# Optimization experiments

Measured on AMD Instinct MI355X. Metric: run time of the kernel, lower is better.

The kernel has to match this reference:

```python
import jax, jax.numpy as jnp
import numpy as np

EPS = 1e-5


def _batchnorm(x, gamma, beta):
    # training-mode BatchNorm over the point/voxel dim (axis 0)
    mean = jnp.mean(x, axis=0)
    var = jnp.var(x, axis=0)
    return (x - mean) * jax.lax.rsqrt(var + EPS) * gamma + beta


def setup_inputs() -> dict:
    N, P, NI, NF, K, I = 100000, 200000, 32, 64, 27, 8
    key = jax.random.key(0)
    ks = jax.random.split(key, 10)
    return {
        "x_feats": jax.random.normal(ks[0], (N, NI), jnp.float32),
        "z_feats": jax.random.normal(ks[1], (P, NI), jnp.float32),
        "interp_w": jax.random.uniform(ks[2], (P, I), jnp.float32),
        "nbr_idx": jax.random.randint(ks[3], (N, K), 0, N, jnp.int32),
        "interp_idx": jax.random.randint(ks[4], (P, I), 0, N, jnp.int32),
        "p2v_idx": jax.random.randint(ks[5], (P,), 0, N, jnp.int32),
        "conv1_w": jax.random.normal(ks[6], (K, NI, NF), jnp.float32) / np.float32(np.sqrt(K * NI)),
        "conv2_w": jax.random.normal(ks[7], (K, NF, NF), jnp.float32) / np.float32(np.sqrt(K * NF)),
        "bn_gamma": jnp.ones((NF,), jnp.float32),
        "bn_beta": jnp.zeros((NF,), jnp.float32),
        "pbn_gamma": jnp.ones((NI,), jnp.float32),
        "pbn_beta": jnp.zeros((NI,), jnp.float32),
        "lin_w": jax.random.normal(ks[8], (NI, NF), jnp.float32) / np.float32(np.sqrt(NI)),
        "lin_b": jnp.zeros((NF,), jnp.float32),
    }


def reference(x_feats, z_feats, interp_w, nbr_idx, interp_idx, p2v_idx,
              conv1_w, conv2_w, bn_gamma, bn_beta, pbn_gamma, pbn_beta,
              lin_w, lin_b):
    N = x_feats.shape[0]
    # --- voxel branch: Conv3d -> BN -> SiLU -> Conv3d (submanifold sparse conv
    # = neighbor gather via kernel map + grouped GEMM over 27 offsets) ---
    h = jnp.einsum('nki,kio->no', x_feats[nbr_idx], conv1_w)   # [N, NF]
    h = jax.nn.silu(_batchnorm(h, bn_gamma, bn_beta))
    x = jnp.einsum('nki,kio->no', h[nbr_idx], conv2_w)         # [N, NF]
    # --- voxel_to_point: trilinear gather from 8 surrounding voxels ---
    z1 = jnp.sum(x[interp_idx] * interp_w[..., None], axis=1)  # [P, NF]
    # --- point branch: z1.F += Linear(SiLU(BN(z.F))) ---
    pz = jax.nn.silu(_batchnorm(z_feats, pbn_gamma, pbn_beta))
    z1 = z1 + pz @ lin_w + lin_b                               # [P, NF]
    # --- point_to_voxel: scatter-average point features into voxels ---
    sums = jax.ops.segment_sum(z1, p2v_idx, num_segments=N)    # [N, NF]
    cnt = jax.ops.segment_sum(jnp.ones((z1.shape[0], 1), z1.dtype), p2v_idx,
                              num_segments=N)
    x_new = sums / jnp.maximum(cnt, 1.0)
    return (x_new, z1)
```

## Files before the change

kernel.cpp:

```cpp
#include <hip/hip_runtime.h>
#include <cstdint>

#define EPSF 1e-5f
constexpr int KOFF = 27;

typedef __attribute__((ext_vector_type(8))) short bf16x8;
typedef __attribute__((ext_vector_type(4))) float f32x4;
typedef unsigned short ushort_t;
typedef unsigned int uint_t;

__device__ __forceinline__ ushort_t f2b(float f) {
    uint_t u = __float_as_uint(f);
    u += 0x7fffu + ((u >> 16) & 1u);
    return (ushort_t)(u >> 16);
}
__device__ __forceinline__ void u4tof(uint4 u, float* f) {
    uint_t w[4] = {u.x, u.y, u.z, u.w};
#pragma unroll
    for (int i = 0; i < 4; ++i) {
        f[2 * i]     = __uint_as_float(w[i] << 16);
        f[2 * i + 1] = __uint_as_float(w[i] & 0xffff0000u);
    }
}

__device__ __forceinline__ void gload_lds16(const void* g, float* l) {
    __builtin_amdgcn_global_load_lds(
        (const __attribute__((address_space(1))) void*)g,
        (__attribute__((address_space(3))) void*)l, 16, 0, 0);
}

__global__ __launch_bounds__(256) void cvt_k(const float* __restrict__ in,
                                             ushort_t* __restrict__ out, int n8) {
    int i = blockIdx.x * 256 + threadIdx.x;
    if (i >= n8) return;
    float4 a = ((const float4*)in)[2 * i];
    float4 b = ((const float4*)in)[2 * i + 1];
    uint4 o;
    o.x = (uint_t)f2b(a.x) | ((uint_t)f2b(a.y) << 16);
    o.y = (uint_t)f2b(a.z) | ((uint_t)f2b(a.w) << 16);
    o.z = (uint_t)f2b(b.x) | ((uint_t)f2b(b.y) << 16);
    o.w = (uint_t)f2b(b.z) | ((uint_t)f2b(b.w) << 16);
    ((uint4*)out)[i] = o;
}

__global__ __launch_bounds__(256) void wtT_k(const float* __restrict__ W,
                                             ushort_t* __restrict__ Wt, int CIN) {
    int t     = blockIdx.x * 256 + threadIdx.x;
    int total = KOFF * CIN * 64;
    if (t >= total) return;
    int o    = t & 63;
    int rest = t >> 6;
    int i    = rest % CIN;
    int k    = rest / CIN;
    Wt[((size_t)k * 64 + o) * CIN + i] = f2b(W[t]);
}

__global__ __launch_bounds__(256) void linT_k(const float* __restrict__ lw,
                                              ushort_t* __restrict__ wt) {
    int t = blockIdx.x * 256 + threadIdx.x;
    if (t >= 64 * 32) return;
    int o = t >> 5, i = t & 31;
    wt[o * 32 + i] = f2b(lw[i * 64 + o]);
}

template <int CIN>
__global__ __launch_bounds__(256, 6) void convm_k(
    const ushort_t* __restrict__ feats,
    const int* __restrict__ nbr,
    const ushort_t* __restrict__ Wt,
    ushort_t* __restrict__ outp,
    int N) {
    constexpr int CHUNKS = CIN / 8;
    constexpr int T      = CIN / 32;
    constexpr int NS     = CHUNKS / 4;
    constexpr int M      = CHUNKS - 1;
    constexpr int PH     = 2;
    constexpr int NPH    = (KOFF + PH - 1) / PH;

    __shared__ float lds[2][PH][64 * CHUNKS * 4];

    const int lane = threadIdx.x & 63;
    const int wv   = threadIdx.x >> 6;
    const int lo   = lane & 15;
    const int hi   = lane >> 4;
    const int row0 = blockIdx.x * 64;

    int srcoff[NS];
    const int* nbp[NS];
    int ldsbase[NS];
#pragma unroll
    for (int i = 0; i < NS; ++i) {
        int c      = (wv * NS + i) * 64 + lane;
        int r      = c / CHUNKS;
        int ch     = c & M;
        srcoff[i]  = (ch ^ (r & M)) * 8;
        int grow   = row0 + r;
        if (grow >= N) grow = N - 1;
        nbp[i]     = nbr + (size_t)grow * KOFF;
        ldsbase[i] = (wv * NS + i) * 256;
    }

    f32x4 acc[4] = {{0.f, 0.f, 0.f, 0.f},
                    {0.f, 0.f, 0.f, 0.f},
                    {0.f, 0.f, 0.f, 0.f},
                    {0.f, 0.f, 0.f, 0.f}};

    int idxb[2][PH][NS];
    bf16x8 Bb[2][PH][T];

    auto NSTEPS = [&](int pp) { return (pp * PH + PH <= KOFF) ? PH : (KOFF - pp * PH); };

    auto LOADIDX = [&](int pp) {
        int ns = NSTEPS(pp);
#pragma unroll
        for (int s = 0; s < PH; ++s)
            if (s < ns)
#pragma unroll
                for (int i = 0; i < NS; ++i)
                    idxb[pp & 1][s][i] = nbp[i][pp * PH + s];
    };
    auto LOADB = [&](int pp) {
        int ns = NSTEPS(pp);
#pragma unroll
        for (int s = 0; s < PH; ++s)
            if (s < ns) {
                const ushort_t* wb =
                    Wt + ((size_t)(pp * PH + s) * 64 + wv * 16 + lo) * CIN + hi * 8;
#pragma unroll
                for (int t = 0; t < T; ++t)
                    Bb[pp & 1][s][t] = *(const bf16x8*)(wb + t * 32);
            }
    };
    auto STAGE = [&](int pp) {
        int ns = NSTEPS(pp);
#pragma unroll
        for (int s = 0; s < PH; ++s)
            if (s < ns)
#pragma unroll
                for (int i = 0; i < NS; ++i) {
                    const ushort_t* src =
                        feats + (size_t)idxb[pp & 1][s][i] * CIN + srcoff[i];
                    gload_lds16(src, &lds[pp & 1][s][ldsbase[i]]);
                }
    };

    LOADIDX(0);
    LOADIDX(1);
    LOADB(0);
    STAGE(0);
    __syncthreads();

#pragma unroll
    for (int p = 0; p < NPH; ++p) {
        if (p + 2 < NPH) LOADIDX(p + 2);
        if (p + 1 < NPH) {
            LOADB(p + 1);
            STAGE(p + 1);
        }
        __builtin_amdgcn_sched_barrier(0);
        int ns = NSTEPS(p);
#pragma unroll
        for (int s = 0; s < PH; ++s) {
            if (s < ns) {
#pragma unroll
                for (int mt = 0; mt < 4; ++mt) {
                    const int R = mt * 16 + lo;
#pragma unroll
                    for (int t = 0; t < T; ++t) {
                        int d    = t * 4 + hi;
                        int slot = d ^ (R & M);
                        bf16x8 a =
                            *(const bf16x8*)&lds[p & 1][s][(R * CHUNKS + slot) * 4];
                        acc[mt] = __builtin_amdgcn_mfma_f32_16x16x32_bf16(
                            a, Bb[p & 1][s][t], acc[mt], 0, 0, 0);
                    }
                }
            }
        }
        __syncthreads();
    }

#pragma unroll
    for (int mt = 0; mt < 4; ++mt) {
#pragma unroll
        for (int r = 0; r < 4; ++r) {
            int orow = row0 + mt * 16 + hi * 4 + r;
            if (orow < N)
                outp[(size_t)orow * 64 + wv * 16 + lo] = f2b(acc[mt][r]);
        }
    }
}

__global__ __launch_bounds__(256) void statsp1_k(const float* __restrict__ v,
                                                 int n, float* __restrict__ part) {
    __shared__ float ls[2 * 256];
    const int c = threadIdx.x & 31;
    int r0      = blockIdx.x * 8 + (threadIdx.x >> 5);
    int stride  = gridDim.x * 8;
    float s = 0.f, ss = 0.f;
    for (int r = r0; r < n; r += stride) {
        float x = v[(size_t)r * 32 + c];
        s += x;
        ss += x * x;
    }
    ls[threadIdx.x]       = s;
    ls[256 + threadIdx.x] = ss;
    __syncthreads();
    for (int off = 128; off >= 32; off >>= 1) {
        if (threadIdx.x < off) {
            ls[threadIdx.x] += ls[threadIdx.x + off];
            ls[256 + threadIdx.x] += ls[256 + threadIdx.x + off];
        }
        __syncthreads();
    }
    if (threadIdx.x < 32) {
        part[(size_t)blockIdx.x * 64 + threadIdx.x]      = ls[threadIdx.x];
        part[(size_t)blockIdx.x * 64 + 32 + threadIdx.x] = ls[256 + threadIdx.x];
    }
}

__global__ __launch_bounds__(256) void statsb1_k(const ushort_t* __restrict__ v,
                                                 int n, float* __restrict__ part) {
    __shared__ float ls[2][256];
    const int c8 = threadIdx.x & 7;
    int r0 = blockIdx.x * 32 + (threadIdx.x >> 3);
    float s[8], ss[8];
#pragma unroll
    for (int j = 0; j < 8; ++j) { s[j] = 0.f; ss[j] = 0.f; }
    for (int r = r0; r < n; r += gridDim.x * 32) {
        uint4 u = *(const uint4*)(v + (size_t)r * 64 + c8 * 8);
        float f[8];
        u4tof(u, f);
#pragma unroll
        for (int j = 0; j < 8; ++j) { s[j] += f[j]; ss[j] += f[j] * f[j]; }
    }
#pragma unroll
    for (int j = 0; j < 8; ++j) {
        ls[0][threadIdx.x] = s[j];
        ls[1][threadIdx.x] = ss[j];
        __syncthreads();
        for (int off = 128; off >= 8; off >>= 1) {
            if (threadIdx.x < off) {
                ls[0][threadIdx.x] += ls[0][threadIdx.x + off];
                ls[1][threadIdx.x] += ls[1][threadIdx.x + off];
            }
            __syncthreads();
        }
        if (threadIdx.x < 8) {
            part[(size_t)blockIdx.x * 128 + threadIdx.x * 8 + j]      = ls[0][threadIdx.x];
            part[(size_t)blockIdx.x * 128 + 64 + threadIdx.x * 8 + j] = ls[1][threadIdx.x];
        }
        __syncthreads();
    }
}

__global__ __launch_bounds__(128) void statsr_k(const float* __restrict__ part,
                                                float* __restrict__ out,
                                                int G, int C2) {
    int c = threadIdx.x;
    if (c >= C2) return;
    float s = 0.f;
#pragma unroll 8
    for (int g = 0; g < G; ++g) s += part[(size_t)g * C2 + c];
    out[c] = s;
}

__global__ __launch_bounds__(256) void bnsilub_k(ushort_t* __restrict__ h,
                                                 const float* __restrict__ stats,
                                                 const float* __restrict__ gamma,
                                                 const float* __restrict__ beta,
                                                 int total8, float invN) {
    int i8 = blockIdx.x * 256 + threadIdx.x;
    if (i8 >= total8) return;
    int c0  = (i8 * 8) & 63;
    uint4 u = ((const uint4*)h)[i8];
    float f[8];
    u4tof(u, f);
#pragma unroll
    for (int j = 0; j < 8; ++j) {
        int c     = c0 + j;
        float m   = stats[c] * invN;
        float var = stats[64 + c] * invN - m * m;
        float x   = (f[j] - m) * rsqrtf(var + EPSF) * gamma[c] + beta[c];
        f[j]      = x / (1.f + expf(-x));
    }
    uint4 o;
    o.x = (uint_t)f2b(f[0]) | ((uint_t)f2b(f[1]) << 16);
    o.y = (uint_t)f2b(f[2]) | ((uint_t)f2b(f[3]) << 16);
    o.z = (uint_t)f2b(f[4]) | ((uint_t)f2b(f[5]) << 16);
    o.w = (uint_t)f2b(f[6]) | ((uint_t)f2b(f[7]) << 16);
    ((uint4*)h)[i8] = o;
}

__global__ __launch_bounds__(256) void point_k(
    const ushort_t* __restrict__ x,
    const float* __restrict__ z_feats,
    const float* __restrict__ interp_w,
    const int* __restrict__ interp_idx,
    const ushort_t* __restrict__ lin_wt,
    const float* __restrict__ lin_b,
    const float* __restrict__ pstats, const float* __restrict__ pgamma,
    const float* __restrict__ pbeta, float* __restrict__ z1_out,
    int P, float invP) {
    __shared__ ushort_t pz[64 * 40];
    __shared__ float zl[64 * 68];

    const int lane = threadIdx.x & 63;
    const int wv   = threadIdx.x >> 6;
    const int lo   = lane & 15;
    const int hi   = lane >> 4;
    const int p0   = blockIdx.x * 64;

    {
        int pp = p0 + lane;
        if (pp >= P) pp = P - 1;
        const int cb      = wv;
        const float4* zr  = (const float4*)(z_feats + (size_t)pp * 32 + cb * 8);
        float4 z0 = zr[0], z1v = zr[1];
        float f[8] = {z0.x, z0.y, z0.z, z0.w, z1v.x, z1v.y, z1v.z, z1v.w};
        uint_t pk[4];
#pragma unroll
        for (int j2 = 0; j2 < 4; ++j2) {
            ushort_t lo16, hi16;
#pragma unroll
            for (int e = 0; e < 2; ++e) {
                int j     = j2 * 2 + e;
                int c     = cb * 8 + j;
                float m   = pstats[c] * invP;
                float var = pstats[32 + c] * invP - m * m;
                float zn  = (f[j] - m) * rsqrtf(var + EPSF) * pgamma[c] + pbeta[c];
                float pzv = zn / (1.f + expf(-zn));
                ushort_t b = f2b(pzv);
                if (e == 0) lo16 = b; else hi16 = b;
            }
            pk[j2] = (uint_t)lo16 | ((uint_t)hi16 << 16);
        }
        *(uint4*)&pz[lane * 40 + cb * 8] = make_uint4(pk[0], pk[1], pk[2], pk[3]);
    }
    __syncthreads();

    {
        bf16x8 a = *(const bf16x8*)&pz[(wv * 16 + lo) * 40 + hi * 8];
        f32x4 lacc[4];
#pragma unroll
        for (int nt = 0; nt < 4; ++nt) {
            bf16x8 b = *(const bf16x8*)(lin_wt + (size_t)(nt * 16 + lo) * 32 + hi * 8);
            lacc[nt] = __builtin_amdgcn_mfma_f32_16x16x32_bf16(
                a, b, (f32x4){0.f, 0.f, 0.f, 0.f}, 0, 0, 0);
        }
#pragma unroll
        for (int nt = 0; nt < 4; ++nt)
#pragma unroll
            for (int r = 0; r < 4; ++r)
                zl[(wv * 16 + hi * 4 + r) * 68 + nt * 16 + lo] = lacc[nt][r];
    }
    __syncthreads();

    const int p = p0 + lane;
    if (p >= P) return;
    const int wbase = __builtin_amdgcn_readfirstlane(wv * 16);

    const int4* iip   = (const int4*)(interp_idx + (size_t)p * 8);
    const float4* iwp = (const float4*)(interp_w + (size_t)p * 8);
    int4 ia = iip[0], ib = iip[1];
    float4 wa = iwp[0], wb = iwp[1];
    int idxs[8]  = {ia.x, ia.y, ia.z, ia.w, ib.x, ib.y, ib.z, ib.w};
    float wts[8] = {wa.x, wa.y, wa.z, wa.w, wb.x, wb.y, wb.z, wb.w};

    float acc[16];
#pragma unroll
    for (int o4 = 0; o4 < 4; ++o4) {
        f32x4 lv = *(const f32x4*)&zl[lane * 68 + wbase + o4 * 4];
#pragma unroll
        for (int j = 0; j < 4; ++j) acc[o4 * 4 + j] = lv[j];
    }

#pragma unroll
    for (int t = 0; t < 8; ++t) {
        const ushort_t* xr = x + (size_t)idxs[t] * 64 + wbase;
        float w            = wts[t];
        uint4 u0 = *(const uint4*)xr;
        uint4 u1 = *(const uint4*)(xr + 8);
        float f[16];
        u4tof(u0, f);
        u4tof(u1, f + 8);
#pragma unroll
        for (int o = 0; o < 16; ++o) acc[o] = fmaf(w, f[o], acc[o]);
    }

    const float* lb = lin_b + wbase;
#pragma unroll
    for (int o = 0; o < 16; ++o) acc[o] += lb[o];

    float* zo = z1_out + (size_t)p * 64 + wbase;
#pragma unroll
    for (int o = 0; o < 16; o += 4) {
        float4 v = {acc[o], acc[o + 1], acc[o + 2], acc[o + 3]};
        *(float4*)(zo + o) = v;
    }
}

__global__ __launch_bounds__(256) void hist_k(const int* __restrict__ p2v,
                                              int* __restrict__ cnt, int P) {
    int p = blockIdx.x * 256 + threadIdx.x;
    if (p < P) atomicAdd(&cnt[p2v[p]], 1);
}

__global__ __launch_bounds__(256) void scan1_k(const int* __restrict__ cnt,
                                               int* __restrict__ tmp,
                                               int* __restrict__ bsum, int n) {
    __shared__ int s[256];
    int i = blockIdx.x * 256 + threadIdx.x;
    int v = (i < n) ? cnt[i] : 0;
    s[threadIdx.x] = v;
    __syncthreads();
    for (int off = 1; off < 256; off <<= 1) {
        int t = (threadIdx.x >= off) ? s[threadIdx.x - off] : 0;
        __syncthreads();
        s[threadIdx.x] += t;
        __syncthreads();
    }
    if (i < n) tmp[i] = s[threadIdx.x];
    if (threadIdx.x == 255) bsum[blockIdx.x] = s[255];
}

__global__ void scan2_k(const int* __restrict__ bsum, int* __restrict__ bpre,
                        int nb) {
    if (blockIdx.x == 0 && threadIdx.x == 0) {
        int a = 0;
        for (int b = 0; b < nb; ++b) { bpre[b] = a; a += bsum[b]; }
    }
}

__global__ __launch_bounds__(256) void scan3_k(const int* __restrict__ cnt,
                                               const int* __restrict__ tmp,
                                               const int* __restrict__ bpre,
                                               int* __restrict__ off, int n) {
    int i = blockIdx.x * 256 + threadIdx.x;
    if (i < n) off[i] = bpre[i >> 8] + tmp[i] - cnt[i];
}

__global__ __launch_bounds__(256) void fill_k(const int* __restrict__ p2v,
                                              const int* __restrict__ off,
                                              int* __restrict__ cursor,
                                              int* __restrict__ bucket, int P) {
    int p = blockIdx.x * 256 + threadIdx.x;
    if (p >= P) return;
    int v    = p2v[p];
    int slot = atomicAdd(&cursor[v], 1);
    bucket[off[v] + slot] = p;
}

__global__ __launch_bounds__(256) void avg_k(const float* __restrict__ z1,
                                             const int* __restrict__ off,
                                             const int* __restrict__ cnt,
                                             const int* __restrict__ bucket,
                                             float* __restrict__ xnew, int N) {
    int tid = blockIdx.x * 256 + threadIdx.x;
    int v   = tid >> 2;
    if (v >= N) return;
    int q  = tid & 3;
    int c  = cnt[v];
    int st = off[v];
    float acc[16];
#pragma unroll
    for (int o = 0; o < 16; ++o) acc[o] = 0.f;
    for (int j = 0; j < c; ++j) {
        int p            = bucket[st + j];
        const float4* zr = (const float4*)(z1 + (size_t)p * 64 + q * 16);
#pragma unroll
        for (int c4 = 0; c4 < 4; ++c4) {
            float4 t = zr[c4];
            acc[c4 * 4 + 0] += t.x;
            acc[c4 * 4 + 1] += t.y;
            acc[c4 * 4 + 2] += t.z;
            acc[c4 * 4 + 3] += t.w;
        }
    }
    float rc  = 1.f / fmaxf((float)c, 1.f);
    float* op = xnew + (size_t)v * 64 + q * 16;
#pragma unroll
    for (int o = 0; o < 16; o += 4) {
        float4 t = {acc[o] * rc, acc[o + 1] * rc, acc[o + 2] * rc, acc[o + 3] * rc};
        *(float4*)(op + o) = t;
    }
}

extern "C" void kernel_launch(void* const* d_in, const int* in_sizes, int n_in,
                              void* d_out, int out_size, void* d_ws, size_t ws_size,
                              hipStream_t stream) {
    const float* x_feats   = (const float*)d_in[0];
    const float* z_feats   = (const float*)d_in[1];
    const float* interp_w  = (const float*)d_in[2];
    const int* nbr_idx     = (const int*)d_in[3];
    const int* interp_idx  = (const int*)d_in[4];
    const int* p2v_idx     = (const int*)d_in[5];
    const float* conv1_w   = (const float*)d_in[6];
    const float* conv2_w   = (const float*)d_in[7];
    const float* bn_gamma  = (const float*)d_in[8];
    const float* bn_beta   = (const float*)d_in[9];
    const float* pbn_gamma = (const float*)d_in[10];
    const float* pbn_beta  = (const float*)d_in[11];
    const float* lin_w     = (const float*)d_in[12];
    const float* lin_b     = (const float*)d_in[13];

    const int N  = in_sizes[3] / KOFF;
    const int P  = in_sizes[5];
    const int NB = (N + 255) / 256;
    const int GH = 512;
    const int GP = 256;

    ushort_t* h2    = (ushort_t*)d_ws;
    ushort_t* xb    = h2 + (size_t)N * 64;
    ushort_t* xf16  = xb + (size_t)N * 64;
    ushort_t* wt1   = xf16 + (size_t)N * 32;
    ushort_t* wt2   = wt1 + KOFF * 64 * 32;
    ushort_t* lwt   = wt2 + KOFF * 64 * 64;
    int* cnt        = (int*)(lwt + 64 * 32);
    int* cursor     = cnt + N;
    float* stats    = (float*)(cursor + N);
    int* tmp        = (int*)(stats + 192);
    int* off        = tmp + N;
    int* bsum       = off + N;
    int* bpre       = bsum + 512;
    int* bucket     = bpre + 512;
    float* part_h   = (float*)(bucket + P);
    float* part_p   = part_h + (size_t)GH * 128;
    float* stats_h  = stats;
    float* stats_p  = stats + 128;

    float* xnew = (float*)d_out;
    float* z1   = xnew + (size_t)N * 64;

    hipMemsetAsync(cnt, 0, (size_t)2 * N * sizeof(int), stream);

    cvt_k<<<((size_t)N * 32 / 8 + 255) / 256, 256, 0, stream>>>(x_feats, xf16,
                                                                N * 32 / 8);
    wtT_k<<<(KOFF * 32 * 64 + 255) / 256, 256, 0, stream>>>(conv1_w, wt1, 32);
    wtT_k<<<(KOFF * 64 * 64 + 255) / 256, 256, 0, stream>>>(conv2_w, wt2, 64);
    linT_k<<<8, 256, 0, stream>>>(lin_w, lwt);

    hist_k<<<(P + 255) / 256, 256, 0, stream>>>(p2v_idx, cnt, P);
    scan1_k<<<NB, 256, 0, stream>>>(cnt, tmp, bsum, N);
    scan2_k<<<1, 1, 0, stream>>>(bsum, bpre, NB);
    scan3_k<<<NB, 256, 0, stream>>>(cnt, tmp, bpre, off, N);
    fill_k<<<(P + 255) / 256, 256, 0, stream>>>(p2v_idx, off, cursor, bucket, P);

    statsp1_k<<<GP, 256, 0, stream>>>(z_feats, P, part_p);
    statsr_k<<<1, 128, 0, stream>>>(part_p, stats_p, GP, 64);

    convm_k<32><<<(N + 63) / 64, 256, 0, stream>>>(xf16, nbr_idx, wt1, h2, N);

    statsb1_k<<<GH, 256, 0, stream>>>(h2, N, part_h);
    statsr_k<<<1, 128, 0, stream>>>(part_h, stats_h, GH, 128);
    bnsilub_k<<<((size_t)N * 64 / 8 + 255) / 256, 256, 0, stream>>>(
        h2, stats_h, bn_gamma, bn_beta, N * 64 / 8, 1.f / (float)N);

    convm_k<64><<<(N + 63) / 64, 256, 0, stream>>>(h2, nbr_idx, wt2, xb, N);

    point_k<<<(P + 63) / 64, 256, 0, stream>>>(xb, z_feats, interp_w, interp_idx,
                                               lwt, lin_b, stats_p, pbn_gamma,
                                               pbn_beta, z1, P, 1.f / (float)P);

    avg_k<<<((size_t)N * 4 + 255) / 256, 256, 0, stream>>>(z1, off, cnt, bucket,
                                                           xnew, N);

    (void)n_in; (void)out_size; (void)ws_size;
}
```

Measured before the change: 313.6 us.

## Enlarge sparse conv tile to 128 rows with 8 waves and parallelize block scan

The sparse conv kernel now processes 128 output rows per block with 512 threads arranged as 2 row groups by 4 column groups. Each staged weight fragment is reused across more rows, and the number of blocks is halved. The single-thread serial scan over block sums becomes a 512-thread shared-memory Hillis-Steele scan, which assumes at most 512 blocks. LDS per block doubles and occupancy limits change, which may reduce the latency hiding available for the gathers.

```diff
diff --git a/kernel.cpp b/kernel.cpp
--- a/kernel.cpp
+++ b/kernel.cpp
@@ -64,7 +64,7 @@
 }
 
 template <int CIN>
-__global__ __launch_bounds__(256, 6) void convm_k(
+__global__ __launch_bounds__(512, 4) void convm_k(
     const ushort_t* __restrict__ feats,
     const int* __restrict__ nbr,
     const ushort_t* __restrict__ Wt,
@@ -77,27 +77,29 @@
     constexpr int PH     = 2;
     constexpr int NPH    = (KOFF + PH - 1) / PH;
 
-    __shared__ float lds[2][PH][64 * CHUNKS * 4];
+    __shared__ float lds[2][PH][128 * CHUNKS * 4];
 
     const int lane = threadIdx.x & 63;
-    const int wv   = threadIdx.x >> 6;
+    const int wid  = threadIdx.x >> 6;
+    const int wr   = wid >> 2;
+    const int wc   = wid & 3;
     const int lo   = lane & 15;
     const int hi   = lane >> 4;
-    const int row0 = blockIdx.x * 64;
+    const int row0 = blockIdx.x * 128;
 
     int srcoff[NS];
     const int* nbp[NS];
     int ldsbase[NS];
 #pragma unroll
     for (int i = 0; i < NS; ++i) {
-        int c      = (wv * NS + i) * 64 + lane;
+        int c      = (wid * NS + i) * 64 + lane;
         int r      = c / CHUNKS;
         int ch     = c & M;
         srcoff[i]  = (ch ^ (r & M)) * 8;
         int grow   = row0 + r;
         if (grow >= N) grow = N - 1;
         nbp[i]     = nbr + (size_t)grow * KOFF;
-        ldsbase[i] = (wv * NS + i) * 256;
+        ldsbase[i] = (wid * NS + i) * 256;
     }
 
     f32x4 acc[4] = {{0.f, 0.f, 0.f, 0.f},
@@ -125,7 +127,7 @@
         for (int s = 0; s < PH; ++s)
             if (s < ns) {
                 const ushort_t* wb =
-                    Wt + ((size_t)(pp * PH + s) * 64 + wv * 16 + lo) * CIN + hi * 8;
+                    Wt + ((size_t)(pp * PH + s) * 64 + wc * 16 + lo) * CIN + hi * 8;
 #pragma unroll
                 for (int t = 0; t < T; ++t)
                     Bb[pp & 1][s][t] = *(const bf16x8*)(wb + t * 32);
@@ -164,7 +166,7 @@
             if (s < ns) {
 #pragma unroll
                 for (int mt = 0; mt < 4; ++mt) {
-                    const int R = mt * 16 + lo;
+                    const int R = wr * 64 + mt * 16 + lo;
 #pragma unroll
                     for (int t = 0; t < T; ++t) {
                         int d    = t * 4 + hi;
@@ -184,9 +186,9 @@
     for (int mt = 0; mt < 4; ++mt) {
 #pragma unroll
         for (int r = 0; r < 4; ++r) {
-            int orow = row0 + mt * 16 + hi * 4 + r;
+            int orow = row0 + wr * 64 + mt * 16 + hi * 4 + r;
             if (orow < N)
-                outp[(size_t)orow * 64 + wv * 16 + lo] = f2b(acc[mt][r]);
+                outp[(size_t)orow * 64 + wc * 16 + lo] = f2b(acc[mt][r]);
         }
     }
 }
@@ -424,12 +426,20 @@
     if (threadIdx.x == 255) bsum[blockIdx.x] = s[255];
 }
 
-__global__ void scan2_k(const int* __restrict__ bsum, int* __restrict__ bpre,
-                        int nb) {
-    if (blockIdx.x == 0 && threadIdx.x == 0) {
-        int a = 0;
-        for (int b = 0; b < nb; ++b) { bpre[b] = a; a += bsum[b]; }
-    }
+__global__ __launch_bounds__(512) void scan2_k(const int* __restrict__ bsum,
+                                               int* __restrict__ bpre, int nb) {
+    __shared__ int s[512];
+    int i = threadIdx.x;
+    int v = (i < nb) ? bsum[i] : 0;
+    s[i]  = v;
+    __syncthreads();
+    for (int off = 1; off < 512; off <<= 1) {
+        int t = (i >= off) ? s[i - off] : 0;
+        __syncthreads();
+        s[i] += t;
+        __syncthreads();
+    }
+    if (i < nb) bpre[i] = s[i] - v;
 }
 
 __global__ __launch_bounds__(256) void scan3_k(const int* __restrict__ cnt,
@@ -542,21 +552,21 @@
 
     hist_k<<<(P + 255) / 256, 256, 0, stream>>>(p2v_idx, cnt, P);
     scan1_k<<<NB, 256, 0, stream>>>(cnt, tmp, bsum, N);
-    scan2_k<<<1, 1, 0, stream>>>(bsum, bpre, NB);
+    scan2_k<<<1, 512, 0, stream>>>(bsum, bpre, NB);
     scan3_k<<<NB, 256, 0, stream>>>(cnt, tmp, bpre, off, N);
     fill_k<<<(P + 255) / 256, 256, 0, stream>>>(p2v_idx, off, cursor, bucket, P);
 
     statsp1_k<<<GP, 256, 0, stream>>>(z_feats, P, part_p);
     statsr_k<<<1, 128, 0, stream>>>(part_p, stats_p, GP, 64);
 
-    convm_k<32><<<(N + 63) / 64, 256, 0, stream>>>(xf16, nbr_idx, wt1, h2, N);
+    convm_k<32><<<(N + 127) / 128, 512, 0, stream>>>(xf16, nbr_idx, wt1, h2, N);
 
     statsb1_k<<<GH, 256, 0, stream>>>(h2, N, part_h);
     statsr_k<<<1, 128, 0, stream>>>(part_h, stats_h, GH, 128);
     bnsilub_k<<<((size_t)N * 64 / 8 + 255) / 256, 256, 0, stream>>>(
         h2, stats_h, bn_gamma, bn_beta, N * 64 / 8, 1.f / (float)N);
 
-    convm_k<64><<<(N + 63) / 64, 256, 0, stream>>>(h2, nbr_idx, wt2, xb, N);
+    convm_k<64><<<(N + 127) / 128, 512, 0, stream>>>(h2, nbr_idx, wt2, xb, N);
 
     point_k<<<(P + 63) / 64, 256, 0, stream>>>(xb, z_feats, interp_w, interp_idx,
                                                lwt, lin_b, stats_p, pbn_gamma,
```

After: 312.3 us. Within noise of the previous version (-0.4%).

## Fuse BN stats into conv1 epilogue, write bucketed bf16 z1, parallelize scan

Applied to the files above, without the earlier changes.

The first sparse conv now accumulates per-channel sum and sum-of-squares in its epilogue and writes per-block partials, which removes the separate stats pass over h2. The point kernel also writes a bf16 copy of z1 directly into voxel-sorted slot order, so avg_k reads contiguous bf16 rows instead of gathering fp32 rows through a bucket index. The single-thread block-prefix scan becomes a 512-thread parallel scan. In exchange the averaged output now sums bf16-rounded values, which lowers precision, and the stats reduction has to go over more partials (one per conv block).

```diff
diff --git a/kernel.cpp b/kernel.cpp
--- a/kernel.cpp
+++ b/kernel.cpp
@@ -13,6 +13,9 @@
     uint_t u = __float_as_uint(f);
     u += 0x7fffu + ((u >> 16) & 1u);
     return (ushort_t)(u >> 16);
+}
+__device__ __forceinline__ float b2f(ushort_t u) {
+    return __uint_as_float(((uint_t)u) << 16);
 }
 __device__ __forceinline__ void u4tof(uint4 u, float* f) {
     uint_t w[4] = {u.x, u.y, u.z, u.w};
@@ -63,12 +66,13 @@
     wt[o * 32 + i] = f2b(lw[i * 64 + o]);
 }
 
-template <int CIN>
+template <int CIN, bool STATS>
 __global__ __launch_bounds__(256, 6) void convm_k(
     const ushort_t* __restrict__ feats,
     const int* __restrict__ nbr,
     const ushort_t* __restrict__ Wt,
     ushort_t* __restrict__ outp,
+    float* __restrict__ part,
     int N) {
     constexpr int CHUNKS = CIN / 8;
     constexpr int T      = CIN / 32;
@@ -180,13 +184,31 @@
         __syncthreads();
     }
 
+    float s = 0.f, ss = 0.f;
 #pragma unroll
     for (int mt = 0; mt < 4; ++mt) {
 #pragma unroll
         for (int r = 0; r < 4; ++r) {
             int orow = row0 + mt * 16 + hi * 4 + r;
-            if (orow < N)
-                outp[(size_t)orow * 64 + wv * 16 + lo] = f2b(acc[mt][r]);
+            if (orow < N) {
+                ushort_t b = f2b(acc[mt][r]);
+                outp[(size_t)orow * 64 + wv * 16 + lo] = b;
+                if (STATS) {
+                    float v = b2f(b);
+                    s += v;
+                    ss += v * v;
+                }
+            }
+        }
+    }
+    if (STATS) {
+        s  += __shfl_xor(s, 16);
+        s  += __shfl_xor(s, 32);
+        ss += __shfl_xor(ss, 16);
+        ss += __shfl_xor(ss, 32);
+        if (hi == 0) {
+            part[(size_t)blockIdx.x * 128 + wv * 16 + lo]      = s;
+            part[(size_t)blockIdx.x * 128 + 64 + wv * 16 + lo] = ss;
         }
     }
 }
@@ -219,41 +241,6 @@
     }
 }
 
-__global__ __launch_bounds__(256) void statsb1_k(const ushort_t* __restrict__ v,
-                                                 int n, float* __restrict__ part) {
-    __shared__ float ls[2][256];
-    const int c8 = threadIdx.x & 7;
-    int r0 = blockIdx.x * 32 + (threadIdx.x >> 3);
-    float s[8], ss[8];
-#pragma unroll
-    for (int j = 0; j < 8; ++j) { s[j] = 0.f; ss[j] = 0.f; }
-    for (int r = r0; r < n; r += gridDim.x * 32) {
-        uint4 u = *(const uint4*)(v + (size_t)r * 64 + c8 * 8);
-        float f[8];
-        u4tof(u, f);
-#pragma unroll
-        for (int j = 0; j < 8; ++j) { s[j] += f[j]; ss[j] += f[j] * f[j]; }
-    }
-#pragma unroll
-    for (int j = 0; j < 8; ++j) {
-        ls[0][threadIdx.x] = s[j];
-        ls[1][threadIdx.x] = ss[j];
-        __syncthreads();
-        for (int off = 128; off >= 8; off >>= 1) {
-            if (threadIdx.x < off) {
-                ls[0][threadIdx.x] += ls[0][threadIdx.x + off];
-                ls[1][threadIdx.x] += ls[1][threadIdx.x + off];
-            }
-            __syncthreads();
-        }
-        if (threadIdx.x < 8) {
-            part[(size_t)blockIdx.x * 128 + threadIdx.x * 8 + j]      = ls[0][threadIdx.x];
-            part[(size_t)blockIdx.x * 128 + 64 + threadIdx.x * 8 + j] = ls[1][threadIdx.x];
-        }
-        __syncthreads();
-    }
-}
-
 __global__ __launch_bounds__(128) void statsr_k(const float* __restrict__ part,
                                                 float* __restrict__ out,
                                                 int G, int C2) {
@@ -300,7 +287,8 @@
     const ushort_t* __restrict__ lin_wt,
     const float* __restrict__ lin_b,
     const float* __restrict__ pstats, const float* __restrict__ pgamma,
-    const float* __restrict__ pbeta, float* __restrict__ z1_out,
+    const float* __restrict__ pbeta, const int* __restrict__ pslot,
+    float* __restrict__ z1_out, ushort_t* __restrict__ z1b,
     int P, float invP) {
     __shared__ ushort_t pz[64 * 40];
     __shared__ float zl[64 * 68];
@@ -398,6 +386,15 @@
         float4 v = {acc[o], acc[o + 1], acc[o + 2], acc[o + 3]};
         *(float4*)(zo + o) = v;
     }
+
+    int ps = pslot[p];
+    uint_t pk[8];
+#pragma unroll
+    for (int j = 0; j < 8; ++j)
+        pk[j] = (uint_t)f2b(acc[2 * j]) | ((uint_t)f2b(acc[2 * j + 1]) << 16);
+    ushort_t* zb = z1b + (size_t)ps * 64 + wbase;
+    *(uint4*)zb       = make_uint4(pk[0], pk[1], pk[2], pk[3]);
+    *(uint4*)(zb + 8) = make_uint4(pk[4], pk[5], pk[6], pk[7]);
 }
 
 __global__ __launch_bounds__(256) void hist_k(const int* __restrict__ p2v,
@@ -424,12 +421,20 @@
     if (threadIdx.x == 255) bsum[blockIdx.x] = s[255];
 }
 
-__global__ void scan2_k(const int* __restrict__ bsum, int* __restrict__ bpre,
-                        int nb) {
-    if (blockIdx.x == 0 && threadIdx.x == 0) {
-        int a = 0;
-        for (int b = 0; b < nb; ++b) { bpre[b] = a; a += bsum[b]; }
-    }
+__global__ __launch_bounds__(512) void scan2_k(const int* __restrict__ bsum,
+                                               int* __restrict__ bpre, int nb) {
+    __shared__ int s[512];
+    int i = threadIdx.x;
+    int v = (i < nb) ? bsum[i] : 0;
+    s[i]  = v;
+    __syncthreads();
+    for (int off = 1; off < 512; off <<= 1) {
+        int t = (i >= off) ? s[i - off] : 0;
+        __syncthreads();
+        s[i] += t;
+        __syncthreads();
+    }
+    if (i < nb) bpre[i] = s[i] - v;
 }
 
 __global__ __launch_bounds__(256) void scan3_k(const int* __restrict__ cnt,
@@ -443,18 +448,17 @@
 __global__ __launch_bounds__(256) void fill_k(const int* __restrict__ p2v,
                                               const int* __restrict__ off,
                                               int* __restrict__ cursor,
-                                              int* __restrict__ bucket, int P) {
+                                              int* __restrict__ pslot, int P) {
     int p = blockIdx.x * 256 + threadIdx.x;
     if (p >= P) return;
     int v    = p2v[p];
     int slot = atomicAdd(&cursor[v], 1);
-    bucket[off[v] + slot] = p;
-}
-
-__global__ __launch_bounds__(256) void avg_k(const float* __restrict__ z1,
+    pslot[p] = off[v] + slot;
+}
+
+__global__ __launch_bounds__(256) void avg_k(const ushort_t* __restrict__ z1b,
                                              const int* __restrict__ off,
                                              const int* __restrict__ cnt,
-                                             const int* __restrict__ bucket,
                                              float* __restrict__ xnew, int N) {
     int tid = blockIdx.x * 256 + threadIdx.x;
     int v   = tid >> 2;
@@ -466,16 +470,14 @@
 #pragma unroll
     for (int o = 0; o < 16; ++o) acc[o] = 0.f;
     for (int j = 0; j < c; ++j) {
-        int p            = bucket[st + j];
-        const float4* zr = (const float4*)(z1 + (size_t)p * 64 + q * 16);
-#pragma unroll
-        for (int c4 = 0; c4 < 4; ++c4) {
-            float4 t = zr[c4];
-            acc[c4 * 4 + 0] += t.x;
-            acc[c4 * 4 + 1] += t.y;
-            acc[c4 * 4 + 2] += t.z;
-            acc[c4 * 4 + 3] += t.w;
-        }
+        const ushort_t* zr = z1b + (size_t)(st + j) * 64 + q * 16;
+        uint4 u0 = *(const uint4*)zr;
+        uint4 u1 = *(const uint4*)(zr + 8);
+        float f[16];
+        u4tof(u0, f);
+        u4tof(u1, f + 8);
+#pragma unroll
+        for (int o = 0; o < 16; ++o) acc[o] += f[o];
     }
     float rc  = 1.f / fmaxf((float)c, 1.f);
     float* op = xnew + (size_t)v * 64 + q * 16;
@@ -507,7 +509,7 @@
     const int N  = in_sizes[3] / KOFF;
     const int P  = in_sizes[5];
     const int NB = (N + 255) / 256;
-    const int GH = 512;
+    const int GC = (N + 63) / 64;
     const int GP = 256;
 
     ushort_t* h2    = (ushort_t*)d_ws;
@@ -523,9 +525,10 @@
     int* off        = tmp + N;
     int* bsum       = off + N;
     int* bpre       = bsum + 512;
-    int* bucket     = bpre + 512;
-    float* part_h   = (float*)(bucket + P);
-    float* part_p   = part_h + (size_t)GH * 128;
+    int* pslot      = bpre + 512;
+    ushort_t* z1b   = (ushort_t*)(pslot + P);
+    float* part_h   = (float*)(z1b + (size_t)P * 64);
+    float* part_p   = part_h + (size_t)GC * 128;
     float* stats_h  = stats;
     float* stats_p  = stats + 128;
 
@@ -542,28 +545,26 @@
 
     hist_k<<<(P + 255) / 256, 256, 0, stream>>>(p2v_idx, cnt, P);
     scan1_k<<<NB, 256, 0, stream>>>(cnt, tmp, bsum, N);
-    scan2_k<<<1, 1, 0, stream>>>(bsum, bpre, NB);
+    scan2_k<<<1, 512, 0, stream>>>(bsum, bpre, NB);
     scan3_k<<<NB, 256, 0, stream>>>(cnt, tmp, bpre, off, N);
-    fill_k<<<(P + 255) / 256, 256, 0, stream>>>(p2v_idx, off, cursor, bucket, P);
+    fill_k<<<(P + 255) / 256, 256, 0, stream>>>(p2v_idx, off, cursor, pslot, P);
 
     statsp1_k<<<GP, 256, 0, stream>>>(z_feats, P, part_p);
     statsr_k<<<1, 128, 0, stream>>>(part_p, stats_p, GP, 64);
 
-    convm_k<32><<<(N + 63) / 64, 256, 0, stream>>>(xf16, nbr_idx, wt1, h2, N);
-
-    statsb1_k<<<GH, 256, 0, stream>>>(h2, N, part_h);
-    statsr_k<<<1, 128, 0, stream>>>(part_h, stats_h, GH, 128);
+    convm_k<32, true><<<GC, 256, 0, stream>>>(xf16, nbr_idx, wt1, h2, part_h, N);
+    statsr_k<<<1, 128, 0, stream>>>(part_h, stats_h, GC, 128);
     bnsilub_k<<<((size_t)N * 64 / 8 + 255) / 256, 256, 0, stream>>>(
         h2, stats_h, bn_gamma, bn_beta, N * 64 / 8, 1.f / (float)N);
 
-    convm_k<64><<<(N + 63) / 64, 256, 0, stream>>>(h2, nbr_idx, wt2, xb, N);
+    convm_k<64, false><<<GC, 256, 0, stream>>>(h2, nbr_idx, wt2, xb, nullptr, N);
 
     point_k<<<(P + 63) / 64, 256, 0, stream>>>(xb, z_feats, interp_w, interp_idx,
                                                lwt, lin_b, stats_p, pbn_gamma,
-                                               pbn_beta, z1, P, 1.f / (float)P);
-
-    avg_k<<<((size_t)N * 4 + 255) / 256, 256, 0, stream>>>(z1, off, cnt, bucket,
-                                                           xnew, N);
+                                               pbn_beta, pslot, z1, z1b,
+                                               P, 1.f / (float)P);
+
+    avg_k<<<((size_t)N * 4 + 255) / 256, 256, 0, stream>>>(z1b, off, cnt, xnew, N);
 
     (void)n_in; (void)out_size; (void)ws_size;
 }
```

After: 327.5 us. 4.4% more time.
